# Performance work log

Hardware: AMD Instinct MI355X
Metric: run time of the kernel (lower is better)

## Reference

```python
import jax, jax.numpy as jnp
import numpy as np

HIDDEN = 2048
N_HEADS = 16
N_KV_HEADS = 4
HEAD_DIM = 128
N_REP = N_HEADS // N_KV_HEADS
BATCH = 2
SEQ = 2048
SCALE = HEAD_DIM ** -0.5
NEG = -1e9


def apply_rope(x, freqs):
    # x: (b, s, h, d); freqs: (s, d//2) angles. Interleaved-pair rotation.
    cos = jnp.cos(freqs)[None, :, None, :]
    sin = jnp.sin(freqs)[None, :, None, :]
    x1 = x[..., 0::2]
    x2 = x[..., 1::2]
    r1 = x1 * cos - x2 * sin
    r2 = x1 * sin + x2 * cos
    return jnp.stack([r1, r2], axis=-1).reshape(x.shape)


def setup_inputs() -> dict:
    key = jax.random.key(0)
    ks = jax.random.split(key, 6)
    x = jax.random.normal(ks[0], (BATCH, SEQ, HIDDEN), dtype=jnp.float32)
    wq = jax.random.normal(ks[1], (N_HEADS * HEAD_DIM, HIDDEN), dtype=jnp.float32) * 0.02
    wk = jax.random.normal(ks[2], (N_KV_HEADS * HEAD_DIM, HIDDEN), dtype=jnp.float32) * 0.02
    wv = jax.random.normal(ks[3], (N_KV_HEADS * HEAD_DIM, HIDDEN), dtype=jnp.float32) * 0.02
    wo = jax.random.normal(ks[4], (HIDDEN, N_HEADS * HEAD_DIM), dtype=jnp.float32) * 0.02
    # RoPE angle table: pos * theta^{-2i/d}
    inv_freq = 1.0 / (10000.0 ** (jnp.arange(0, HEAD_DIM, 2, dtype=jnp.float32) / HEAD_DIM))
    rope_freqs = jnp.arange(SEQ, dtype=jnp.float32)[:, None] * inv_freq[None, :]  # (S, d/2)
    # additive causal mask
    causal = jnp.tril(jnp.ones((SEQ, SEQ), dtype=bool))
    mask = jnp.where(causal, 0.0, NEG).astype(jnp.float32)[None, None]  # (1,1,S,S)
    return {"x": x, "wq": wq, "wk": wk, "wv": wv, "wo": wo,
            "rope_freqs": rope_freqs, "mask": mask}


def reference(x, wq, wk, wv, wo, rope_freqs, mask):
    b, s, _ = x.shape
    q = (x @ wq.T).reshape(b, s, N_HEADS, HEAD_DIM)
    k = (x @ wk.T).reshape(b, s, N_KV_HEADS, HEAD_DIM)
    v = (x @ wv.T).reshape(b, s, N_KV_HEADS, HEAD_DIM)
    q = apply_rope(q, rope_freqs)
    k = apply_rope(k, rope_freqs)
    new_k, new_v = k, v  # kv cache (no prior cache, start_pos=0)
    # GQA: repeat each kv head n_rep times (matches expand+reshape in source)
    k_rep = jnp.repeat(k, N_REP, axis=2)  # (b, s, n_heads, d)
    v_rep = jnp.repeat(v, N_REP, axis=2)
    scores = jnp.einsum('bqhd,bkhd->bhqk', q, k_rep) * SCALE
    scores = scores + mask
    attn = jax.nn.softmax(scores.astype(jnp.float32), axis=-1).astype(q.dtype)
    out = jnp.einsum('bhqk,bkhd->bqhd', attn, v_rep).reshape(b, s, -1)
    return out @ wo.T, (new_k, new_v)
```

## Files before the change

kernel.cpp:

```cpp
#include <hip/hip_runtime.h>
#include <hip/hip_bf16.h>

#define NH 16
#define NKV 4
#define HD 128
#define QSCALE 0.1275174272f

using bf16x8 = __attribute__((ext_vector_type(8))) __bf16;
using f32x4  = __attribute__((ext_vector_type(4))) float;
using u16x8  = __attribute__((ext_vector_type(8))) unsigned short;
using u16x2  = __attribute__((ext_vector_type(2))) unsigned short;

__device__ __forceinline__ unsigned short f2b(float f) {
  __hip_bfloat16 h = __float2bfloat16(f);
  return __builtin_bit_cast(unsigned short, h);
}
__device__ __forceinline__ float b2f(unsigned short u) {
  unsigned int v = ((unsigned int)u) << 16;
  return __builtin_bit_cast(float, v);
}

__device__ __forceinline__ void glds16(const unsigned short* g, unsigned short* l) {
  __builtin_amdgcn_global_load_lds(
      (const __attribute__((address_space(1))) unsigned int*)(const void*)g,
      (__attribute__((address_space(3))) unsigned int*)(void*)l, 16, 0, 0);
}

__global__ __launch_bounds__(256) void cvt_fused(const float* __restrict__ x,
                                                 const float* __restrict__ wq,
                                                 const float* __restrict__ wk,
                                                 const float* __restrict__ wv,
                                                 const float* __restrict__ wo,
                                                 unsigned short* __restrict__ xb,
                                                 unsigned short* __restrict__ wqkvb,
                                                 unsigned short* __restrict__ wob) {
  int i = blockIdx.x * 256 + threadIdx.x;
  const float* src;
  unsigned short* dst;
  int off;
  if (i < 1048576)      { src = x;  dst = xb;              off = i; }
  else if (i < 1572864) { src = wq; dst = wqkvb;           off = i - 1048576; }
  else if (i < 1703936) { src = wk; dst = wqkvb + 4194304; off = i - 1572864; }
  else if (i < 1835008) { src = wv; dst = wqkvb + 5242880; off = i - 1703936; }
  else                  { src = wo; dst = wob;             off = i - 1835008; }
  const float4* s4 = reinterpret_cast<const float4*>(src) + (size_t)off * 2;
  float4 v0 = s4[0], v1 = s4[1];
  u16x8 o;
  o[0] = f2b(v0.x); o[1] = f2b(v0.y); o[2] = f2b(v0.z); o[3] = f2b(v0.w);
  o[4] = f2b(v1.x); o[5] = f2b(v1.y); o[6] = f2b(v1.z); o[7] = f2b(v1.w);
  reinterpret_cast<u16x8*>(dst)[off] = o;
}

template<int CF32>
__global__ __launch_bounds__(512, 1) void gemm256(const unsigned short* __restrict__ A,
                                                  const unsigned short* __restrict__ B,
                                                  void* __restrict__ C,
                                                  int N, int K, int nbx) {
  __shared__ unsigned short As[3 * 8192];
  __shared__ unsigned short Bs[3 * 8192];
  const int tid = threadIdx.x, lane = tid & 63;
  const int wid = tid >> 6, wm = wid >> 2, wn = wid & 3;
  const int cpx = gridDim.x >> 3;
  const int wgid = (blockIdx.x & 7) * cpx + (blockIdx.x >> 3);
  const int bx = wgid % nbx, by = wgid / nbx;
  const int row0 = by * 256, col0 = bx * 256;
  const int fr = lane & 15, g = lane >> 4;
  const int NT = K >> 5;

  size_t offA[2], offB[2];
#pragma unroll
  for (int l = 0; l < 2; l++) {
    int cid = tid + l * 512, R = cid >> 3, phys = cid & 7, cl = phys ^ (R & 7);
    int row = 2 * R + (cl >> 2), kc = cl & 3;
    offA[l] = (size_t)(row0 + row) * K + kc * 8;
    offB[l] = (size_t)(col0 + row) * K + kc * 8;
  }

  auto stage_half = [&](int t, int sb, int h) {
    int k0 = t * 32;
    glds16(A + offA[h] + k0, &As[sb * 8192 + (tid + h * 512) * 8]);
    glds16(B + offB[h] + k0, &Bs[sb * 8192 + (tid + h * 512) * 8]);
  };

  auto ldfrag = [&](const unsigned short* buf, int row) {
    int R = row >> 1;
    int phys = ((((row & 1) << 2) | g) ^ (R & 7));
    return *reinterpret_cast<const bf16x8*>(&buf[R * 64 + phys * 8]);
  };

  f32x4 acc[8][4];
#pragma unroll
  for (int i = 0; i < 8; i++)
#pragma unroll
    for (int j = 0; j < 4; j++) acc[i][j] = f32x4{0.f, 0.f, 0.f, 0.f};

  stage_half(0, 0, 0); stage_half(0, 0, 1);
  stage_half(1, 1, 0); stage_half(1, 1, 1);
  asm volatile("s_waitcnt vmcnt(4)" ::: "memory");
  __builtin_amdgcn_s_barrier();
  __builtin_amdgcn_sched_barrier(0);

  int rb = 0, sb = 2;
#pragma unroll 1
  for (int t = 0; t < NT; ++t) {
    const unsigned short* Ar = &As[rb * 8192];
    const unsigned short* Br = &Bs[rb * 8192];

    bf16x8 bfr[4], a[4];
#pragma unroll
    for (int nf = 0; nf < 4; nf++) bfr[nf] = ldfrag(Br, wn * 64 + nf * 16 + fr);
#pragma unroll
    for (int mf = 0; mf < 4; mf++) a[mf] = ldfrag(Ar, wm * 128 + mf * 16 + fr);
    if (t + 2 < NT) stage_half(t + 2, sb, 0);
    __builtin_amdgcn_s_barrier();
    asm volatile("s_waitcnt lgkmcnt(0)" ::: "memory");
    __builtin_amdgcn_sched_barrier(0);
    __builtin_amdgcn_s_setprio(1);
#pragma unroll
    for (int mf = 0; mf < 4; mf++)
#pragma unroll
      for (int nf = 0; nf < 4; nf++)
        acc[mf][nf] = __builtin_amdgcn_mfma_f32_16x16x32_bf16(a[mf], bfr[nf], acc[mf][nf], 0, 0, 0);
    __builtin_amdgcn_s_setprio(0);
    __builtin_amdgcn_sched_barrier(0);
    __builtin_amdgcn_s_barrier();

    bf16x8 a2[4];
#pragma unroll
    for (int mf = 0; mf < 4; mf++) a2[mf] = ldfrag(Ar, wm * 128 + (mf + 4) * 16 + fr);
    if (t + 2 < NT) stage_half(t + 2, sb, 1);
    __builtin_amdgcn_s_barrier();
    asm volatile("s_waitcnt lgkmcnt(0)" ::: "memory");
    __builtin_amdgcn_sched_barrier(0);
    __builtin_amdgcn_s_setprio(1);
#pragma unroll
    for (int mf = 0; mf < 4; mf++)
#pragma unroll
      for (int nf = 0; nf < 4; nf++)
        acc[mf + 4][nf] = __builtin_amdgcn_mfma_f32_16x16x32_bf16(a2[mf], bfr[nf], acc[mf + 4][nf], 0, 0, 0);
    __builtin_amdgcn_s_setprio(0);
    __builtin_amdgcn_sched_barrier(0);

    if (t + 1 < NT) {
      if (t + 2 < NT) asm volatile("s_waitcnt vmcnt(4)" ::: "memory");
      else            asm volatile("s_waitcnt vmcnt(0)" ::: "memory");
      __builtin_amdgcn_s_barrier();
      __builtin_amdgcn_sched_barrier(0);
    }
    rb = rb == 2 ? 0 : rb + 1;
    sb = sb == 2 ? 0 : sb + 1;
  }

#pragma unroll
  for (int i = 0; i < 8; i++) {
#pragma unroll
    for (int j = 0; j < 4; j++) {
      int rbase = row0 + wm * 128 + i * 16 + g * 4;
      int cb = col0 + wn * 64 + j * 16 + fr;
#pragma unroll
      for (int r = 0; r < 4; r++) {
        if (CF32)
          reinterpret_cast<float*>(C)[(size_t)(rbase + r) * N + cb] = acc[i][j][r];
        else
          reinterpret_cast<unsigned short*>(C)[(size_t)(rbase + r) * N + cb] = f2b(acc[i][j][r]);
      }
    }
  }
}

__global__ __launch_bounds__(256) void rope_kernel(const unsigned short* __restrict__ qkv,
                                                   const float* __restrict__ freqs,
                                                   unsigned short* __restrict__ qro,
                                                   unsigned short* __restrict__ kro,
                                                   float* __restrict__ newk) {
  const int NQ = 4096 * 16 * 64;
  const int NK = 4096 * 4 * 64;
  int idx = blockIdx.x * 256 + threadIdx.x;
  if (idx >= NQ + NK) return;
  if (idx < NQ) {
    int i = idx & 63;
    int h = (idx >> 6) & 15;
    int row = idx >> 10;
    int s = row & 2047, b = row >> 11;
    float f = freqs[s * 64 + i];
    float c = cosf(f), sn = sinf(f);
    u16x2 xv = *reinterpret_cast<const u16x2*>(qkv + (size_t)row * 3072 + h * 128 + 2 * i);
    float x1 = b2f(xv.x), x2 = b2f(xv.y);
    float r1 = (x1 * c - x2 * sn) * QSCALE;
    float r2 = (x1 * sn + x2 * c) * QSCALE;
    u16x2 o; o.x = f2b(r1); o.y = f2b(r2);
    *reinterpret_cast<u16x2*>(qro + ((size_t)(b * 16 + h) * 2048 + s) * 128 + 2 * i) = o;
  } else {
    idx -= NQ;
    int i = idx & 63;
    int h = (idx >> 6) & 3;
    int row = idx >> 8;
    int s = row & 2047, b = row >> 11;
    float f = freqs[s * 64 + i];
    float c = cosf(f), sn = sinf(f);
    u16x2 xv = *reinterpret_cast<const u16x2*>(qkv + (size_t)row * 3072 + 2048 + h * 128 + 2 * i);
    float x1 = b2f(xv.x), x2 = b2f(xv.y);
    float r1 = x1 * c - x2 * sn;
    float r2 = x1 * sn + x2 * c;
    u16x2 o; o.x = f2b(r1); o.y = f2b(r2);
    *reinterpret_cast<u16x2*>(kro + ((size_t)(b * 4 + h) * 2048 + s) * 128 + 2 * i) = o;
    float2 of; of.x = r1; of.y = r2;
    *reinterpret_cast<float2*>(newk + (size_t)row * 512 + h * 128 + 2 * i) = of;
  }
}

__global__ __launch_bounds__(256) void vtrans_kernel(const unsigned short* __restrict__ qkv,
                                                     unsigned short* __restrict__ vt,
                                                     float* __restrict__ newv) {
  __shared__ unsigned short T[32][136];
  const int st = blockIdx.x;
  const int kvh = blockIdx.y & 3, b = blockIdx.y >> 2;
  const int s0 = st * 32;
  const int t = threadIdx.x;
  const int ls = t >> 3;
  const int ch = (t & 7) * 2;
  const unsigned short* src = qkv + (size_t)(b * 2048 + s0 + ls) * 3072 + 2560 + kvh * 128 + ch * 8;
  u16x8 a0 = *reinterpret_cast<const u16x8*>(src);
  u16x8 a1 = *reinterpret_cast<const u16x8*>(src + 8);
  *reinterpret_cast<u16x8*>(&T[ls][ch * 8])     = a0;
  *reinterpret_cast<u16x8*>(&T[ls][ch * 8 + 8]) = a1;
  float* nv = newv + (size_t)(b * 2048 + s0 + ls) * 512 + kvh * 128 + ch * 8;
  float4 f0, f1, f2, f3;
  f0.x = b2f(a0[0]); f0.y = b2f(a0[1]); f0.z = b2f(a0[2]); f0.w = b2f(a0[3]);
  f1.x = b2f(a0[4]); f1.y = b2f(a0[5]); f1.z = b2f(a0[6]); f1.w = b2f(a0[7]);
  f2.x = b2f(a1[0]); f2.y = b2f(a1[1]); f2.z = b2f(a1[2]); f2.w = b2f(a1[3]);
  f3.x = b2f(a1[4]); f3.y = b2f(a1[5]); f3.z = b2f(a1[6]); f3.w = b2f(a1[7]);
  reinterpret_cast<float4*>(nv)[0] = f0;
  reinterpret_cast<float4*>(nv)[1] = f1;
  reinterpret_cast<float4*>(nv)[2] = f2;
  reinterpret_cast<float4*>(nv)[3] = f3;
  __syncthreads();
  const int d = t >> 1, half = t & 1;
  unsigned short* dst = vt + ((size_t)(b * 4 + kvh) * 128 + d) * 2048 + s0 + half * 16;
  u16x8 o0, o1;
#pragma unroll
  for (int q = 0; q < 8; q++) {
    int slot = half * 16 + q;
    int kl = ((slot >> 2) & 1) * 16 + (slot >> 3) * 4 + (slot & 3);
    o0[q] = T[kl][d];
  }
#pragma unroll
  for (int q = 0; q < 8; q++) {
    int slot = half * 16 + 8 + q;
    int kl = ((slot >> 2) & 1) * 16 + (slot >> 3) * 4 + (slot & 3);
    o1[q] = T[kl][d];
  }
  reinterpret_cast<u16x8*>(dst)[0] = o0;
  reinterpret_cast<u16x8*>(dst)[1] = o1;
}

__global__ __launch_bounds__(256, 4) void attn_kernel(const unsigned short* __restrict__ qro,
                                                      const unsigned short* __restrict__ kro,
                                                      const unsigned short* __restrict__ vt,
                                                      unsigned short* __restrict__ out) {
  __shared__ unsigned short Ks[2][32 * 128];
  __shared__ unsigned short Vs[2][64 * 64];
  const int tid = threadIdx.x, lane = tid & 63, w = tid >> 6;
  const int kvhb = blockIdx.x & 7;
  const int kvh = kvhb & 3, b = kvhb >> 2;
  const int t = 127 - (blockIdx.x >> 3);
  const int h = kvh * 4 + w;
  const int qbase = t * 16;
  const int fr = lane & 15, g = lane >> 4, fk = g * 8;
  const unsigned short* Kp = kro + (size_t)(b * 4 + kvh) * 2048 * 128;
  const unsigned short* Vtp = vt + (size_t)(b * 4 + kvh) * 128 * 2048;
  const unsigned short* Qp = qro + ((size_t)(b * 16 + h) * 2048 + qbase) * 128;

  bf16x8 qf[4];
#pragma unroll
  for (int kk = 0; kk < 4; kk++)
    qf[kk] = *reinterpret_cast<const bf16x8*>(Qp + fr * 128 + kk * 32 + fk);

  u16x8 onesu;
#pragma unroll
  for (int j = 0; j < 8; j++) onesu[j] = 0x3F80;
  bf16x8 ones = __builtin_bit_cast(bf16x8, onesu);

  f32x4 o[8];
#pragma unroll
  for (int dt = 0; dt < 8; dt++) o[dt] = f32x4{0.f, 0.f, 0.f, 0.f};
  f32x4 dacc = f32x4{0.f, 0.f, 0.f, 0.f};
  const int qrow_s = qbase + fr;
  const int nfull = (qbase >= 31) ? ((qbase - 31) >> 5) + 1 : 0;
  const int niter = nfull + 1;

  const int krow = w * 8 + (lane >> 4);
  const int kcol = lane & 15;
  const int vrow = w * 16 + (lane >> 3);
  const int vcol = lane & 7;

  auto stage = [&](int kv0, int buf) {
    unsigned short* Kb = &Ks[buf][0];
    unsigned short* Vb = &Vs[buf][0];
#pragma unroll
    for (int j = 0; j < 2; j++) {
      int r = krow + j * 4;
      glds16(Kp + (size_t)(kv0 + r) * 128 + ((kcol ^ (r & 7)) * 8),
             Kb + (w * 8 + j * 4) * 128);
    }
#pragma unroll
    for (int j = 0; j < 2; j++) {
      int r = vrow + j * 8;
      int u = vcol ^ (r & 7);
      int d = 2 * r + (u >> 2);
      glds16(Vtp + (size_t)d * 2048 + kv0 + (u & 3) * 8,
             Vb + (w * 16 + j * 8) * 64);
    }
  };

  auto step = [&](int kv0, bool mask, int buf) {
    const unsigned short* Kb = &Ks[buf][0];
    const unsigned short* Vb = &Vs[buf][0];
    f32x4 sc[2];
    sc[0] = sc[1] = f32x4{0.f, 0.f, 0.f, 0.f};
    __builtin_amdgcn_s_setprio(1);
#pragma unroll
    for (int kk = 0; kk < 4; kk++) {
      int blk = ((kk * 4 + g) ^ (fr & 7)) * 8;
      bf16x8 ka0 = *reinterpret_cast<const bf16x8*>(Kb + (fr +  0) * 128 + blk);
      bf16x8 ka1 = *reinterpret_cast<const bf16x8*>(Kb + (fr + 16) * 128 + blk);
      sc[0] = __builtin_amdgcn_mfma_f32_16x16x32_bf16(ka0, qf[kk], sc[0], 0, 0, 0);
      sc[1] = __builtin_amdgcn_mfma_f32_16x16x32_bf16(ka1, qf[kk], sc[1], 0, 0, 0);
    }
    __builtin_amdgcn_s_setprio(0);
#pragma unroll
    for (int s = 0; s < 2; s++)
#pragma unroll
      for (int r = 0; r < 4; r++) {
        float v = sc[s][r];
        if (mask && (kv0 + 16 * s + 4 * g + r > qrow_s)) v = -1e30f;
        sc[s][r] = __builtin_amdgcn_exp2f(v);
      }
    u16x8 pau;
#pragma unroll
    for (int j = 0; j < 4; j++) {
      pau[j]     = f2b(sc[0][j]);
      pau[4 + j] = f2b(sc[1][j]);
    }
    bf16x8 pa = __builtin_bit_cast(bf16x8, pau);
    dacc = __builtin_amdgcn_mfma_f32_16x16x32_bf16(pa, ones, dacc, 0, 0, 0);
    __builtin_amdgcn_s_setprio(1);
#pragma unroll
    for (int dt = 0; dt < 8; dt++) {
      int jr = dt * 8 + (fr >> 1);
      int c = ((fr & 1) * 4 + g) ^ (fr >> 1);
      bf16x8 vf = *reinterpret_cast<const bf16x8*>(Vb + jr * 64 + c * 8);
      o[dt] = __builtin_amdgcn_mfma_f32_16x16x32_bf16(pa, vf, o[dt], 0, 0, 0);
    }
    __builtin_amdgcn_s_setprio(0);
  };

  stage(0, 0);
  int buf = 0;
  for (int i = 0; i < niter; i++) {
    __syncthreads();
    if (i + 1 < niter) stage((i + 1) * 32, buf ^ 1);
    step(i * 32, i == nfull, buf);
    buf ^= 1;
  }

#pragma unroll
  for (int r = 0; r < 4; r++) {
    float inv = 1.0f / dacc[r];
    int qrow = qbase + g * 4 + r;
    size_t rowoff = ((size_t)b * 2048 + qrow) * 2048 + (size_t)h * 128;
#pragma unroll
    for (int dt = 0; dt < 8; dt++)
      out[rowoff + dt * 16 + fr] = f2b(o[dt][r] * inv);
  }
}

extern "C" void kernel_launch(void* const* d_in, const int* in_sizes, int n_in,
                              void* d_out, int out_size, void* d_ws, size_t ws_size,
                              hipStream_t stream) {
  const float* x  = (const float*)d_in[0];
  const float* wq = (const float*)d_in[1];
  const float* wk = (const float*)d_in[2];
  const float* wv = (const float*)d_in[3];
  const float* wo = (const float*)d_in[4];
  const float* freqs = (const float*)d_in[5];

  char* ws = (char*)d_ws;
  unsigned short* xb    = (unsigned short*)(ws);
  unsigned short* attn  = xb;
  unsigned short* wqkvb = (unsigned short*)(ws + 16777216);
  unsigned short* wob   = (unsigned short*)(ws + 29360128);
  unsigned short* qkv   = (unsigned short*)(ws + 37748736);
  unsigned short* qro   = (unsigned short*)(ws + 62914560);
  unsigned short* kro   = (unsigned short*)(ws + 79691776);
  unsigned short* vt    = (unsigned short*)(ws + 83886080);

  float* out_o = (float*)d_out;
  float* out_k = (float*)d_out + 8388608;
  float* out_v = (float*)d_out + 10485760;

  cvt_fused<<<9216, 256, 0, stream>>>(x, wq, wk, wv, wo, xb, wqkvb, wob);

  gemm256<0><<<192, 512, 0, stream>>>(xb, wqkvb, qkv, 3072, 2048, 12);

  rope_kernel<<<20480, 256, 0, stream>>>(qkv, freqs, qro, kro, out_k);
  vtrans_kernel<<<dim3(64, 8), 256, 0, stream>>>(qkv, vt, out_v);

  attn_kernel<<<1024, 256, 0, stream>>>(qro, kro, vt, attn);

  gemm256<1><<<128, 512, 0, stream>>>(attn, wob, out_o, 2048, 2048, 8);
}
```

Measured before the change: 222.1 us.

## Restructure GEMM to K=64 tiles with double-buffered LDS and staggered A/B prefetch

The GEMM kernel moves from a triple-buffered pipeline with 32-wide K tiles to a double-buffered one with 64-wide K tiles. The inner loop is split into four quarter-steps. A for the next tile and B for the tile after that are prefetched in halves during those steps. The aim is to halve the number of outer iterations and barrier/waitcnt rounds and get more MFMA work per LDS fragment load. In exchange, LDS use per block rises (2x2x32KB = 128KB), there are more barriers per iteration, and the prefetch distance for A is shorter.

```diff
diff --git a/kernel.cpp b/kernel.cpp
--- a/kernel.cpp
+++ b/kernel.cpp
@@ -52,12 +52,12 @@
 }
 
 template<int CF32>
-__global__ __launch_bounds__(512, 1) void gemm256(const unsigned short* __restrict__ A,
-                                                  const unsigned short* __restrict__ B,
-                                                  void* __restrict__ C,
-                                                  int N, int K, int nbx) {
-  __shared__ unsigned short As[3 * 8192];
-  __shared__ unsigned short Bs[3 * 8192];
+__global__ __launch_bounds__(512, 1) void gemm_q(const unsigned short* __restrict__ A,
+                                                 const unsigned short* __restrict__ B,
+                                                 void* __restrict__ C,
+                                                 int N, int K, int nbx) {
+  __shared__ unsigned short As[2][256 * 64];
+  __shared__ unsigned short Bs[2][256 * 64];
   const int tid = threadIdx.x, lane = tid & 63;
   const int wid = tid >> 6, wm = wid >> 2, wn = wid & 3;
   const int cpx = gridDim.x >> 3;
@@ -65,90 +65,94 @@
   const int bx = wgid % nbx, by = wgid / nbx;
   const int row0 = by * 256, col0 = bx * 256;
   const int fr = lane & 15, g = lane >> 4;
-  const int NT = K >> 5;
-
-  size_t offA[2], offB[2];
-#pragma unroll
-  for (int l = 0; l < 2; l++) {
-    int cid = tid + l * 512, R = cid >> 3, phys = cid & 7, cl = phys ^ (R & 7);
-    int row = 2 * R + (cl >> 2), kc = cl & 3;
-    offA[l] = (size_t)(row0 + row) * K + kc * 8;
-    offB[l] = (size_t)(col0 + row) * K + kc * 8;
-  }
-
-  auto stage_half = [&](int t, int sb, int h) {
-    int k0 = t * 32;
-    glds16(A + offA[h] + k0, &As[sb * 8192 + (tid + h * 512) * 8]);
-    glds16(B + offB[h] + k0, &Bs[sb * 8192 + (tid + h * 512) * 8]);
+  const int NT = K >> 6;
+
+  size_t offA[2][2], offB[2][2];
+#pragma unroll
+  for (int h = 0; h < 2; h++)
+#pragma unroll
+    for (int l = 0; l < 2; l++) {
+      int cid = h * 1024 + l * 512 + tid;
+      int row = cid >> 3, phys = cid & 7, cl = phys ^ (row & 7);
+      offA[h][l] = (size_t)(row0 + row) * K + cl * 8;
+      offB[h][l] = (size_t)(col0 + row) * K + cl * 8;
+    }
+
+  auto stA = [&](int t, int h) {
+    int k0 = t * 64, sb = t & 1;
+    glds16(A + offA[h][0] + k0, &As[sb][(h * 1024 + tid) * 8]);
+    glds16(A + offA[h][1] + k0, &As[sb][(h * 1024 + 512 + tid) * 8]);
   };
-
-  auto ldfrag = [&](const unsigned short* buf, int row) {
-    int R = row >> 1;
-    int phys = ((((row & 1) << 2) | g) ^ (R & 7));
-    return *reinterpret_cast<const bf16x8*>(&buf[R * 64 + phys * 8]);
+  auto stB = [&](int t, int h) {
+    int k0 = t * 64, sb = t & 1;
+    glds16(B + offB[h][0] + k0, &Bs[sb][(h * 1024 + tid) * 8]);
+    glds16(B + offB[h][1] + k0, &Bs[sb][(h * 1024 + 512 + tid) * 8]);
   };
 
+  auto ldfrag = [&](const unsigned short* buf, int row, int ks) {
+    int phys = ((ks << 2) | g) ^ (row & 7);
+    return *reinterpret_cast<const bf16x8*>(&buf[row * 64 + phys * 8]);
+  };
+
   f32x4 acc[8][4];
 #pragma unroll
   for (int i = 0; i < 8; i++)
 #pragma unroll
     for (int j = 0; j < 4; j++) acc[i][j] = f32x4{0.f, 0.f, 0.f, 0.f};
 
-  stage_half(0, 0, 0); stage_half(0, 0, 1);
-  stage_half(1, 1, 0); stage_half(1, 1, 1);
+  stA(0, 0); stA(0, 1);
+  stB(0, 0); stB(0, 1);
+  stB(1, 0); stB(1, 1);
   asm volatile("s_waitcnt vmcnt(4)" ::: "memory");
   __builtin_amdgcn_s_barrier();
   __builtin_amdgcn_sched_barrier(0);
 
-  int rb = 0, sb = 2;
 #pragma unroll 1
   for (int t = 0; t < NT; ++t) {
-    const unsigned short* Ar = &As[rb * 8192];
-    const unsigned short* Br = &Bs[rb * 8192];
-
-    bf16x8 bfr[4], a[4];
-#pragma unroll
-    for (int nf = 0; nf < 4; nf++) bfr[nf] = ldfrag(Br, wn * 64 + nf * 16 + fr);
-#pragma unroll
-    for (int mf = 0; mf < 4; mf++) a[mf] = ldfrag(Ar, wm * 128 + mf * 16 + fr);
-    if (t + 2 < NT) stage_half(t + 2, sb, 0);
-    __builtin_amdgcn_s_barrier();
-    asm volatile("s_waitcnt lgkmcnt(0)" ::: "memory");
-    __builtin_amdgcn_sched_barrier(0);
-    __builtin_amdgcn_s_setprio(1);
-#pragma unroll
-    for (int mf = 0; mf < 4; mf++)
-#pragma unroll
-      for (int nf = 0; nf < 4; nf++)
-        acc[mf][nf] = __builtin_amdgcn_mfma_f32_16x16x32_bf16(a[mf], bfr[nf], acc[mf][nf], 0, 0, 0);
-    __builtin_amdgcn_s_setprio(0);
-    __builtin_amdgcn_sched_barrier(0);
-    __builtin_amdgcn_s_barrier();
-
-    bf16x8 a2[4];
-#pragma unroll
-    for (int mf = 0; mf < 4; mf++) a2[mf] = ldfrag(Ar, wm * 128 + (mf + 4) * 16 + fr);
-    if (t + 2 < NT) stage_half(t + 2, sb, 1);
-    __builtin_amdgcn_s_barrier();
-    asm volatile("s_waitcnt lgkmcnt(0)" ::: "memory");
-    __builtin_amdgcn_sched_barrier(0);
-    __builtin_amdgcn_s_setprio(1);
-#pragma unroll
-    for (int mf = 0; mf < 4; mf++)
-#pragma unroll
-      for (int nf = 0; nf < 4; nf++)
-        acc[mf + 4][nf] = __builtin_amdgcn_mfma_f32_16x16x32_bf16(a2[mf], bfr[nf], acc[mf + 4][nf], 0, 0, 0);
-    __builtin_amdgcn_s_setprio(0);
-    __builtin_amdgcn_sched_barrier(0);
-
+    const int rb = t & 1;
+    const unsigned short* Ar = &As[rb][0];
+    const unsigned short* Br = &Bs[rb][0];
+    bf16x8 bfr[4][2];
+#pragma unroll
+    for (int q = 0; q < 4; ++q) {
+      bf16x8 a[2][2];
+#pragma unroll
+      for (int i = 0; i < 2; ++i) {
+        int row = wm * 128 + (2 * q + i) * 16 + fr;
+        a[i][0] = ldfrag(Ar, row, 0);
+        a[i][1] = ldfrag(Ar, row, 1);
+      }
+      if (q == 0) {
+#pragma unroll
+        for (int nf = 0; nf < 4; ++nf) {
+          int row = wn * 64 + nf * 16 + fr;
+          bfr[nf][0] = ldfrag(Br, row, 0);
+          bfr[nf][1] = ldfrag(Br, row, 1);
+        }
+      }
+      if (q < 2)  { if (t + 1 < NT) stA(t + 1, q); }
+      else        { if (t + 2 < NT) stB(t + 2, q - 2); }
+      __builtin_amdgcn_s_barrier();
+      asm volatile("s_waitcnt lgkmcnt(0)" ::: "memory");
+      __builtin_amdgcn_sched_barrier(0);
+      __builtin_amdgcn_s_setprio(1);
+#pragma unroll
+      for (int i = 0; i < 2; ++i)
+#pragma unroll
+        for (int nf = 0; nf < 4; ++nf) {
+          acc[2 * q + i][nf] = __builtin_amdgcn_mfma_f32_16x16x32_bf16(a[i][0], bfr[nf][0], acc[2 * q + i][nf], 0, 0, 0);
+          acc[2 * q + i][nf] = __builtin_amdgcn_mfma_f32_16x16x32_bf16(a[i][1], bfr[nf][1], acc[2 * q + i][nf], 0, 0, 0);
+        }
+      __builtin_amdgcn_s_setprio(0);
+      __builtin_amdgcn_sched_barrier(0);
+      __builtin_amdgcn_s_barrier();
+    }
     if (t + 1 < NT) {
       if (t + 2 < NT) asm volatile("s_waitcnt vmcnt(4)" ::: "memory");
       else            asm volatile("s_waitcnt vmcnt(0)" ::: "memory");
       __builtin_amdgcn_s_barrier();
       __builtin_amdgcn_sched_barrier(0);
     }
-    rb = rb == 2 ? 0 : rb + 1;
-    sb = sb == 2 ? 0 : sb + 1;
   }
 
 #pragma unroll
@@ -401,12 +405,12 @@
 
   cvt_fused<<<9216, 256, 0, stream>>>(x, wq, wk, wv, wo, xb, wqkvb, wob);
 
-  gemm256<0><<<192, 512, 0, stream>>>(xb, wqkvb, qkv, 3072, 2048, 12);
+  gemm_q<0><<<192, 512, 0, stream>>>(xb, wqkvb, qkv, 3072, 2048, 12);
 
   rope_kernel<<<20480, 256, 0, stream>>>(qkv, freqs, qro, kro, out_k);
   vtrans_kernel<<<dim3(64, 8), 256, 0, stream>>>(qkv, vt, out_v);
 
   attn_kernel<<<1024, 256, 0, stream>>>(qro, kro, vt, attn);
 
-  gemm256<1><<<128, 512, 0, stream>>>(attn, wob, out_o, 2048, 2048, 8);
-}
+  gemm_q<1><<<128, 512, 0, stream>>>(attn, wob, out_o, 2048, 2048, 8);
+}
```

After: 216.3 us. 2.6% less time.
